# Optimization experiments

Measured on AMD Instinct MI355X. Metric: run time of the kernel, lower is better.

## Reference

```python
import jax, jax.numpy as jnp
import numpy as np

VOCAB, WORD_DIM, EMBED_SIZE, TENSOR_DIM, B = 100000, 300, 1024, 100, 16384

def leaky_relu(x):
    return jnp.where(x >= 0, x, 0.1 * x)

def setup_inputs() -> dict:
    key = jax.random.key(0)
    ks = jax.random.split(key, 12)
    H = EMBED_SIZE // 2
    def unif(k, shape, r):
        return jax.random.uniform(k, shape, jnp.float32, -r, r)
    def xavier_r(fan_in, fan_out):
        return float(np.sqrt(6.0) / np.sqrt(fan_in + fan_out))
    return {
        "x": jax.random.randint(ks[0], (B, 2), 0, VOCAB, dtype=jnp.int64) if jax.config.jax_enable_x64 else jax.random.randint(ks[0], (B, 2), 0, VOCAB, dtype=jnp.int32),
        "lengths": jnp.full((B,), 2, dtype=jnp.int32),
        "embed_W": unif(ks[1], (VOCAB, WORD_DIM), 0.1),
        "pd_W": unif(ks[2], (TENSOR_DIM, WORD_DIM), xavier_r(WORD_DIM, TENSOR_DIM)),
        "pd_b": jnp.zeros((TENSOR_DIM,), jnp.float32),
        "comp_T": jax.random.normal(ks[3], (TENSOR_DIM, 2 * TENSOR_DIM, 2 * TENSOR_DIM), jnp.float32),
        "cl_W": unif(ks[4], (TENSOR_DIM, 2 * TENSOR_DIM), xavier_r(2 * TENSOR_DIM, TENSOR_DIM)),
        "cl_b": jnp.zeros((TENSOR_DIM,), jnp.float32),
        "l1_W": unif(ks[5], (H, TENSOR_DIM), xavier_r(TENSOR_DIM, H)),
        "l1_b": jnp.zeros((H,), jnp.float32),
        "l2_W": unif(ks[6], (EMBED_SIZE, H), xavier_r(H, EMBED_SIZE)),
        "l2_b": jnp.zeros((EMBED_SIZE,), jnp.float32),
    }

def reference(x, lengths, embed_W, pd_W, pd_b, comp_T, cl_W, cl_b, l1_W, l1_b, l2_W, l2_b):
    # embedding lookup + projdown + leaky relu for att (x[:,0]) and obj (x[:,1])
    att = leaky_relu(embed_W[x[:, 0]] @ pd_W.T + pd_b)   # [B, T]
    obj = leaky_relu(embed_W[x[:, 1]] @ pd_W.T + pd_b)   # [B, T]
    cat = jnp.concatenate([att, obj], axis=1)            # [B, 2T]
    # fused trilinear form: cat^T . comp_T[k] . cat for all k at once
    term1 = jnp.einsum('bi,kij,bj->bk', cat, comp_T, cat)  # [B, T]
    term2 = cat @ cl_W.T + cl_b                            # [B, T]
    comp_vec = leaky_relu(term1 + term2)
    out = leaky_relu(comp_vec @ l1_W.T + l1_b) @ l2_W.T + l2_b  # [B, E]
    # l2norm over dim 1
    norm = jnp.sqrt(jnp.sum(out * out, axis=1, keepdims=True))
    return out / norm
```

## Files before the change

kernel.cpp:

```cpp
#include <hip/hip_runtime.h>
#include <hip/hip_bf16.h>

#define BATCH 16384
#define WDIM 300
#define TDIM 100
#define TD2 200
#define HDIM 512
#define ESIZE 1024

#define NIT 13
#define NJC 7
#define CSTR 232
#define CVSTR 136
#define HSTR 520

typedef unsigned short ush;
typedef float f32x2 __attribute__((ext_vector_type(2)));
typedef float f32x4 __attribute__((ext_vector_type(4)));
typedef _Float16 f16x8 __attribute__((ext_vector_type(8)));
typedef _Float16 f16x4 __attribute__((ext_vector_type(4)));

__device__ __forceinline__ float bf2f(ush u) {
    union { unsigned int i; float f; } v; v.i = ((unsigned int)u) << 16; return v.f;
}
__device__ __forceinline__ float2 bf2x2(unsigned int w) {
    union { unsigned int i; float f; } a, b;
    a.i = w << 16; b.i = w & 0xffff0000u;
    return make_float2(a.f, b.f);
}
__device__ __forceinline__ ush f2bf(float f) {
    union { float f; unsigned int i; } v; v.f = f;
    unsigned int x = v.i;
    return (ush)((x + 0x7fffu + ((x >> 16) & 1u)) >> 16);
}
__device__ __forceinline__ float leaky(float v) { return v >= 0.f ? v : 0.1f * v; }

__global__ __launch_bounds__(256) void kA3(const int* __restrict__ x,
                                           const float* __restrict__ eW,
                                           const float* __restrict__ pdW,
                                           const float* __restrict__ pdb,
                                           float* __restrict__ cat)
{
    __shared__ float eS[32][308];
    __shared__ float pS[20][308];
    __shared__ int idxS[32];
    const int tid = threadIdx.x;
    const int lane = tid & 63, wv = tid >> 6;
    const int b0 = blockIdx.x * 16;

    if (tid < 32) idxS[tid] = x[b0 * 2 + tid];
    __syncthreads();

    for (int r = wv; r < 32; r += 4) {
        const float4* src = (const float4*)(eW + (size_t)idxS[r] * WDIM);
        for (int d = lane; d < 75; d += 64) *(float4*)&eS[r][d * 4] = src[d];
    }

    const int r = tid >> 3, tl = tid & 7;
    const int t2ok = (tl + 16) < 20;
    const int b = b0 + (r >> 1), h = r & 1;

    for (int tc = 0; tc < 5; ++tc) {
        __syncthreads();
        for (int i = tid; i < 1500; i += 256) {
            int rr = i / 75, d = i - rr * 75;
            *(float4*)&pS[rr][d * 4] =
                *(const float4*)&pdW[(size_t)(tc * 20 + rr) * WDIM + d * 4];
        }
        __syncthreads();

        float a0 = 0.f, a1 = 0.f, a2 = 0.f;
        const int t2i = t2ok ? (tl + 16) : 0;
        for (int d = 0; d < 75; ++d) {
            float4 e4 = *(const float4*)&eS[r][d * 4];
            float4 p0 = *(const float4*)&pS[tl][d * 4];
            float4 p1 = *(const float4*)&pS[tl + 8][d * 4];
            float4 p2 = *(const float4*)&pS[t2i][d * 4];
            a0 += e4.x * p0.x + e4.y * p0.y + e4.z * p0.z + e4.w * p0.w;
            a1 += e4.x * p1.x + e4.y * p1.y + e4.z * p1.z + e4.w * p1.w;
            a2 += e4.x * p2.x + e4.y * p2.y + e4.z * p2.z + e4.w * p2.w;
        }
        {
            int t = tc * 20 + tl;
            cat[(size_t)b * TD2 + h * 100 + t] = leaky(a0 + pdb[t]);
            t += 8;
            cat[(size_t)b * TD2 + h * 100 + t] = leaky(a1 + pdb[t]);
            if (t2ok) {
                t += 8;
                cat[(size_t)b * TD2 + h * 100 + t] = leaky(a2 + pdb[t]);
            }
        }
    }
}

__global__ __launch_bounds__(448) void kT(const float* __restrict__ compT,
                                          const float* __restrict__ clW,
                                          ush* __restrict__ Tp)
{
    const int k = blockIdx.x, it = blockIdx.y;
    const int jc = threadIdx.x >> 6, lane = threadIdx.x & 63;
    const int i = it * 16 + (lane & 15);
    const int j0 = jc * 32 + (lane >> 4) * 8;
    ush vals[8];
    #pragma unroll
    for (int e = 0; e < 8; ++e) {
        int j = j0 + e;
        float v = 0.f;
        if (j < 200) {
            if (i < 200) v = compT[((size_t)k * 200 + i) * 200 + j];
            else if (i == 200) v = clW[(size_t)k * 200 + j];
        }
        union { _Float16 h; ush u; } cvt; cvt.h = (_Float16)v; vals[e] = cvt.u;
    }
    size_t o = (((size_t)k * NIT + it) * NJC + jc) * 64 + lane;
    ((uint4*)Tp)[o] = *(const uint4*)vals;
}

__global__ __launch_bounds__(256) void kW(const float* __restrict__ l1W,
                                          const float* __restrict__ l2W,
                                          ush* __restrict__ l1p,
                                          ush* __restrict__ l2p)
{
    const int idx = blockIdx.x * 256 + threadIdx.x;
    union { _Float16 h; ush u; } cvt;
    if (idx < HDIM * 128) {
        int r = idx >> 7, c = idx & 127;
        cvt.h = (_Float16)(c < TDIM ? l1W[r * TDIM + c] : 0.f);
        l1p[idx] = cvt.u;
    } else {
        int j = idx - HDIM * 128;
        cvt.h = (_Float16)l2W[j];
        l2p[j] = cvt.u;
    }
}

template<int NT>
__device__ __forceinline__ void kb7_work(const _Float16 (*__restrict__ cS)[CSTR],
                                         float (*__restrict__ pRed)[64],
                                         const ush* __restrict__ Tp,
                                         const float* __restrict__ clb,
                                         float* __restrict__ cv,
                                         int t0, int b0, int lane, int tid)
{
    const int cl = lane & 15, rg = lane >> 4;

    float cval[NT][4][4];
    #pragma unroll
    for (int it = 0; it < NT; ++it)
        #pragma unroll
        for (int bt = 0; bt < 4; ++bt)
            #pragma unroll
            for (int r = 0; r < 4; ++r)
                cval[it][bt][r] = (float)cS[bt * 16 + cl][(t0 + it) * 16 + rg * 4 + r];

    for (int k = 0; k < TDIM; ++k) {
        const int p = k & 1;
        f32x4 acc[NT][4];
        #pragma unroll
        for (int it = 0; it < NT; ++it)
            #pragma unroll
            for (int bt = 0; bt < 4; ++bt)
                acc[it][bt] = (f32x4){0.f, 0.f, 0.f, 0.f};

        #pragma unroll
        for (int jc = 0; jc < NJC; ++jc) {
            f16x8 ah[NT];
            #pragma unroll
            for (int it = 0; it < NT; ++it)
                ah[it] = *(const f16x8*)(Tp +
                    ((((size_t)k * NIT + (t0 + it)) * NJC + jc) * 64 + lane) * 8);
            f16x8 bh[4];
            #pragma unroll
            for (int bt = 0; bt < 4; ++bt)
                bh[bt] = *(const f16x8*)&cS[bt * 16 + cl][jc * 32 + rg * 8];
            #pragma unroll
            for (int it = 0; it < NT; ++it)
                #pragma unroll
                for (int bt = 0; bt < 4; ++bt)
                    acc[it][bt] = __builtin_amdgcn_mfma_f32_16x16x32_f16(
                        ah[it], bh[bt], acc[it][bt], 0, 0, 0);
        }
        #pragma unroll
        for (int bt = 0; bt < 4; ++bt) {
            float v = 0.f;
            #pragma unroll
            for (int it = 0; it < NT; ++it)
                #pragma unroll
                for (int r = 0; r < 4; ++r)
                    v += acc[it][bt][r] * cval[it][bt][r];
            v += __shfl_xor(v, 16);
            v += __shfl_xor(v, 32);
            if (lane < 16) atomicAdd(&pRed[p][bt * 16 + lane], v);
        }
        __syncthreads();
        if (tid < 64) {
            float s = pRed[p][tid];
            pRed[p][tid] = 0.f;
            cv[(size_t)k * BATCH + b0 + tid] = leaky(s + clb[k]);
        }
    }
}

__global__ __launch_bounds__(512, 2) void kB7(const float* __restrict__ cat,
                                              const ush* __restrict__ Tp,
                                              const float* __restrict__ clb,
                                              float* __restrict__ cv)
{
    __shared__ _Float16 cS[64][CSTR];
    __shared__ float pRed[2][64];
    const int tid = threadIdx.x;
    const int b0 = blockIdx.x * 64;
    const int lane = tid & 63, w = tid >> 6;

    for (int idx = tid; idx < 64 * CSTR; idx += 512) {
        int r = idx / CSTR, c = idx - r * CSTR;
        float v = 0.f;
        if (c < 200) v = cat[(size_t)(b0 + r) * TD2 + c];
        else if (c == 200) v = 1.f;
        cS[r][c] = (_Float16)v;
    }
    if (tid < 128) ((float*)pRed)[tid] = 0.f;
    __syncthreads();

    if (w < 5) kb7_work<2>(cS, pRed, Tp, clb, cv, 2 * w, b0, lane, tid);
    else       kb7_work<1>(cS, pRed, Tp, clb, cv, 10 + (w - 5), b0, lane, tid);
}

__global__ __launch_bounds__(512, 2) void kC1(const float* __restrict__ cv,
                                              const ush* __restrict__ l1p,
                                              const float* __restrict__ l1b,
                                              ush* __restrict__ h)
{
    __shared__ _Float16 cvS[64][CVSTR];
    const int tid = threadIdx.x;
    const int b0 = blockIdx.x * 64;
    const int lane = tid & 63, w = tid >> 6;
    const int cl = lane & 15, rg = lane >> 4;

    for (int k0 = 0; k0 < 128; k0 += 8) {
        int k = k0 + (w);
        int bl = lane;
        float v = (k < TDIM) ? cv[(size_t)k * BATCH + b0 + bl] : 0.f;
        cvS[bl][k] = (_Float16)v;
    }
    __syncthreads();

    for (int e8 = 0; e8 < 4; ++e8) {
        const int et = w * 4 + e8;
        f32x4 acc[4];
        #pragma unroll
        for (int bt = 0; bt < 4; ++bt) acc[bt] = (f32x4){0.f, 0.f, 0.f, 0.f};
        #pragma unroll
        for (int kc = 0; kc < 4; ++kc) {
            f16x8 a = *(const f16x8*)((const _Float16*)l1p +
                       (size_t)(et * 16 + cl) * 128 + kc * 32 + rg * 8);
            #pragma unroll
            for (int bt = 0; bt < 4; ++bt) {
                f16x8 b = *(const f16x8*)&cvS[bt * 16 + cl][kc * 32 + rg * 8];
                acc[bt] = __builtin_amdgcn_mfma_f32_16x16x32_f16(a, b, acc[bt], 0, 0, 0);
            }
        }
        float4 bias = *(const float4*)&l1b[et * 16 + rg * 4];
        #pragma unroll
        for (int bt = 0; bt < 4; ++bt) {
            f16x4 hv;
            hv[0] = (_Float16)leaky(acc[bt][0] + bias.x);
            hv[1] = (_Float16)leaky(acc[bt][1] + bias.y);
            hv[2] = (_Float16)leaky(acc[bt][2] + bias.z);
            hv[3] = (_Float16)leaky(acc[bt][3] + bias.w);
            *(f16x4*)((_Float16*)h + (size_t)(b0 + bt * 16 + cl) * HDIM
                      + et * 16 + rg * 4) = hv;
        }
    }
}

__global__ __launch_bounds__(512, 2) void kC2(const ush* __restrict__ h,
                                              const ush* __restrict__ l2p,
                                              const float* __restrict__ l2b,
                                              float* __restrict__ out,
                                              float* __restrict__ ssqg)
{
    __shared__ _Float16 hS[64][HSTR];
    __shared__ float ssqS[64];
    const int tid = threadIdx.x;
    const int b0 = blockIdx.x * 64;
    const int lane = tid & 63, w = tid >> 6;
    const int cl = lane & 15, rg = lane >> 4;

    for (int it = 0; it < 8; ++it) {
        int idx = it * 512 + tid;
        int row = idx >> 6, c8 = (idx & 63) * 8;
        *(uint4*)&hS[row][c8] = *(const uint4*)(h + (size_t)(b0 + row) * HDIM + c8);
    }
    if (tid < 64) ssqS[tid] = 0.f;
    __syncthreads();

    float ssqp[4] = {0.f, 0.f, 0.f, 0.f};
    for (int e8 = 0; e8 < 8; ++e8) {
        const int et = w * 8 + e8;
        f32x4 acc[4];
        #pragma unroll
        for (int bt = 0; bt < 4; ++bt) acc[bt] = (f32x4){0.f, 0.f, 0.f, 0.f};
        #pragma unroll
        for (int kc = 0; kc < 16; ++kc) {
            f16x8 a = *(const f16x8*)((const _Float16*)l2p +
                       (size_t)(et * 16 + cl) * HDIM + kc * 32 + rg * 8);
            #pragma unroll
            for (int bt = 0; bt < 4; ++bt) {
                f16x8 b = *(const f16x8*)&hS[bt * 16 + cl][kc * 32 + rg * 8];
                acc[bt] = __builtin_amdgcn_mfma_f32_16x16x32_f16(a, b, acc[bt], 0, 0, 0);
            }
        }
        float4 bias = *(const float4*)&l2b[et * 16 + rg * 4];
        #pragma unroll
        for (int bt = 0; bt < 4; ++bt) {
            float4 o;
            o.x = acc[bt][0] + bias.x;
            o.y = acc[bt][1] + bias.y;
            o.z = acc[bt][2] + bias.z;
            o.w = acc[bt][3] + bias.w;
            ssqp[bt] += o.x * o.x + o.y * o.y + o.z * o.z + o.w * o.w;
            *(float4*)&out[(size_t)(b0 + bt * 16 + cl) * ESIZE + et * 16 + rg * 4] = o;
        }
    }
    #pragma unroll
    for (int bt = 0; bt < 4; ++bt) {
        float s = ssqp[bt];
        s += __shfl_xor(s, 16);
        s += __shfl_xor(s, 32);
        if (lane < 16) atomicAdd(&ssqS[bt * 16 + lane], s);
    }
    __syncthreads();
    if (tid < 64) ssqg[b0 + tid] = ssqS[tid];
}

__global__ __launch_bounds__(512, 6) void kB4(const float* __restrict__ cat,
                                              const float* __restrict__ compT,
                                              const float* __restrict__ clW,
                                              const float* __restrict__ clb,
                                              float* __restrict__ cv)
{
    __shared__ float cS[64][201];
    const int tid = threadIdx.x;
    const int b0 = blockIdx.x * 64;
    const int lane = tid & 63;
    const int wid = tid >> 6;

    {
        int r = tid / TD2;
        int c = tid - r * TD2;
        for (int i = tid; i < 64 * TD2; i += 512) {
            cS[r][c] = cat[(size_t)(b0 + r) * TD2 + c];
            c += 112;
            if (c >= TD2) { c -= TD2; r += 3; } else { r += 2; }
        }
    }
    __syncthreads();

    int k = blockIdx.y * 8 + wid;
    if (k >= TDIM) return;
    k = __builtin_amdgcn_readfirstlane(k);

    const float* T = compT + (size_t)k * (TD2 * TD2);
    float s = 0.f;
    for (int ch = 0; ch < 4; ++ch) {
        const int c0 = ch * 50;
        f32x2 cj2[25];
        #pragma unroll
        for (int j = 0; j < 25; ++j) {
            f32x2 c2; c2.x = cS[lane][c0 + 2 * j]; c2.y = cS[lane][c0 + 2 * j + 1];
            cj2[j] = c2;
        }
        for (int i = 0; i < TD2; ++i) {
            const f32x2* T2 = (const f32x2*)(T + (size_t)i * TD2 + c0);
            f32x2 trow[25];
            #pragma unroll
            for (int j = 0; j < 25; ++j) trow[j] = T2[j];
            f32x2 u2; u2.x = 0.f; u2.y = 0.f;
            #pragma unroll
            for (int j = 0; j < 25; ++j) {
                asm("v_pk_fma_f32 %0, %1, %2, %0"
                    : "+v"(u2) : "s"(trow[j]), "v"(cj2[j]));
            }
            s += cS[lane][i] * (u2.x + u2.y);
        }
    }
    float t2 = 0.f;
    const float* W = clW + (size_t)k * TD2;
    for (int j = 0; j < TD2; ++j) t2 += W[j] * cS[lane][j];
    cv[(size_t)k * BATCH + b0 + lane] = leaky(s + t2 + clb[k]);
}

__global__ __launch_bounds__(256) void kCf(const float* __restrict__ cv,
                                           const float* __restrict__ l1W,
                                           const float* __restrict__ l1b,
                                           const float* __restrict__ l2W,
                                           const float* __restrict__ l2b,
                                           float* __restrict__ out,
                                           float* __restrict__ ssqg)
{
    __shared__ ush hS[32 * 528];
    __shared__ float w2F[8 * 516];
    const int tid = threadIdx.x;
    const int b0 = blockIdx.x * 32;

    float* cvS = w2F;
    for (int i = tid; i < 3200; i += 256) {
        int k = i >> 5, bl = i & 31;
        cvS[bl * TDIM + k] = cv[(size_t)k * BATCH + b0 + bl];
    }
    __syncthreads();
    for (int o = tid; o < 32 * HDIM; o += 256) {
        int bl = o & 31, e = o >> 5;
        const float* cr = &cvS[bl * TDIM];
        const float* wr = &l1W[e * TDIM];
        float s = 0.f;
        for (int t = 0; t < TDIM; t += 4) {
            float4 w4 = *(const float4*)&wr[t];
            float4 c4 = *(const float4*)&cr[t];
            s += w4.x * c4.x + w4.y * c4.y + w4.z * c4.z + w4.w * c4.w;
        }
        s = leaky(s + l1b[e]);
        hS[bl * 528 + e] = f2bf(s);
    }
    __syncthreads();

    const int b = tid >> 3, el = tid & 7;
    float ssq = 0.f;
    for (int ec = 0; ec < 128; ++ec) {
        {
            const float* src = l2W + (size_t)ec * 8 * HDIM;
            for (int i = tid; i < 1024; i += 256) {
                int r = i >> 7, c4 = (i & 127) * 4;
                *(float4*)&w2F[r * 516 + c4] = *(const float4*)&src[r * HDIM + c4];
            }
        }
        __syncthreads();
        {
            const ush* hr = &hS[b * 528];
            const float* wr2 = &w2F[el * 516];
            float s = 0.f;
            for (int j = 0; j < HDIM; j += 8) {
                uint4 hv = *(const uint4*)&hr[j];
                float4 w0 = *(const float4*)&wr2[j];
                float4 w1 = *(const float4*)&wr2[j + 4];
                float2 h0 = bf2x2(hv.x), h1 = bf2x2(hv.y), h2 = bf2x2(hv.z), h3 = bf2x2(hv.w);
                s += h0.x * w0.x + h0.y * w0.y + h1.x * w0.z + h1.y * w0.w
                   + h2.x * w1.x + h2.y * w1.y + h3.x * w1.z + h3.y * w1.w;
            }
            int eg = ec * 8 + el;
            float v = s + l2b[eg];
            out[(size_t)(b0 + b) * ESIZE + eg] = v;
            ssq += v * v;
        }
        __syncthreads();
    }
    ssq += __shfl_xor(ssq, 1);
    ssq += __shfl_xor(ssq, 2);
    ssq += __shfl_xor(ssq, 4);
    if (el == 0) ssqg[b0 + b] = ssq;
}

__global__ __launch_bounds__(256) void kD(float* __restrict__ out,
                                          const float* __restrict__ ssqg)
{
    const int tid = threadIdx.x;
    const int row = blockIdx.x * 2 + (tid >> 7);
    const int col = (tid & 127) * 8;
    const float r = rsqrtf(ssqg[row]);
    float* p = out + (size_t)row * ESIZE + col;
    float4 v0 = *(float4*)p;
    float4 v1 = *(float4*)(p + 4);
    v0.x *= r; v0.y *= r; v0.z *= r; v0.w *= r;
    v1.x *= r; v1.y *= r; v1.z *= r; v1.w *= r;
    *(float4*)p = v0;
    *(float4*)(p + 4) = v1;
}

extern "C" void kernel_launch(void* const* d_in, const int* in_sizes, int n_in,
                              void* d_out, int out_size, void* d_ws, size_t ws_size,
                              hipStream_t stream) {
    const int*   x    = (const int*)d_in[0];
    const float* eW   = (const float*)d_in[2];
    const float* pdW  = (const float*)d_in[3];
    const float* pdb  = (const float*)d_in[4];
    const float* cT   = (const float*)d_in[5];
    const float* clW  = (const float*)d_in[6];
    const float* clb  = (const float*)d_in[7];
    const float* l1W  = (const float*)d_in[8];
    const float* l1b  = (const float*)d_in[9];
    const float* l2W  = (const float*)d_in[10];
    const float* l2b  = (const float*)d_in[11];
    float* out = (float*)d_out;

    const size_t catN = (size_t)BATCH * TD2;
    const size_t cvN  = (size_t)BATCH * TDIM;
    const size_t ssqN = (size_t)BATCH;
    const size_t tpN  = (size_t)TDIM * NIT * NJC * 64 * 8;
    const size_t l1pN = (size_t)HDIM * 128;
    const size_t l2pN = (size_t)ESIZE * HDIM;
    const size_t hN   = (size_t)BATCH * HDIM;

    float* cat  = (float*)d_ws;
    float* cv   = cat + catN;
    float* ssqg = cv + cvN;
    ush*   Tp   = (ush*)(ssqg + ssqN);
    ush*   l1p  = Tp + tpN;
    ush*   l2p  = l1p + l1pN;
    ush*   hbuf = l2p + l2pN;

    const size_t need = (catN + cvN + ssqN) * 4 + (tpN + l1pN + l2pN + hN) * 2;

    kA3<<<dim3(BATCH / 16), dim3(256), 0, stream>>>(x, eW, pdW, pdb, cat);
    if (ws_size >= need) {
        kT <<<dim3(TDIM, NIT), dim3(448), 0, stream>>>(cT, clW, Tp);
        kW <<<dim3((HDIM * 128 + ESIZE * HDIM) / 256), dim3(256), 0, stream>>>(l1W, l2W, l1p, l2p);
        kB7<<<dim3(BATCH / 64), dim3(512), 0, stream>>>(cat, Tp, clb, cv);
        kC1<<<dim3(BATCH / 64), dim3(512), 0, stream>>>(cv, l1p, l1b, hbuf);
        kC2<<<dim3(BATCH / 64), dim3(512), 0, stream>>>(hbuf, l2p, l2b, out, ssqg);
    } else {
        kB4<<<dim3(BATCH / 64, 13), dim3(512), 0, stream>>>(cat, cT, clW, clb, cv);
        kCf<<<dim3(512), dim3(256), 0, stream>>>(cv, l1W, l1b, l2W, l2b, out, ssqg);
    }
    kD<<<dim3(8192), dim3(256), 0, stream>>>(out, ssqg);
}
```

Measured before the change: 846.2 us.

## Split trilinear kernel over k halves with partial-sum buffer and separate reduction

The bilinear kernel now splits the 100 output k-values between two blocks per batch tile. Within each block, warps are arranged as four i-tile groups times two k-lanes. Each warp writes its per-group partial sums to a global buffer, replacing the per-k shared-memory atomics and block-wide syncs. A new small kernel sums the four partials, adds the bias and applies leaky relu. Launch bounds rise to 4 blocks per SM for more occupancy, at the cost of a 26MB partial buffer round-trip, an extra launch, and cat values reread from LDS instead of held in registers.

```diff
diff --git a/kernel.cpp b/kernel.cpp
--- a/kernel.cpp
+++ b/kernel.cpp
@@ -135,26 +135,17 @@
 }
 
 template<int NT>
-__device__ __forceinline__ void kb7_work(const _Float16 (*__restrict__ cS)[CSTR],
-                                         float (*__restrict__ pRed)[64],
+__device__ __forceinline__ void kb8_work(const _Float16 (*__restrict__ cS)[CSTR],
                                          const ush* __restrict__ Tp,
-                                         const float* __restrict__ clb,
-                                         float* __restrict__ cv,
-                                         int t0, int b0, int lane, int tid)
+                                         float* __restrict__ part,
+                                         int t0, int q, int kq, int klane,
+                                         int b0, int lane)
 {
     const int cl = lane & 15, rg = lane >> 4;
-
-    float cval[NT][4][4];
-    #pragma unroll
-    for (int it = 0; it < NT; ++it)
-        #pragma unroll
-        for (int bt = 0; bt < 4; ++bt)
-            #pragma unroll
-            for (int r = 0; r < 4; ++r)
-                cval[it][bt][r] = (float)cS[bt * 16 + cl][(t0 + it) * 16 + rg * 4 + r];
-
-    for (int k = 0; k < TDIM; ++k) {
-        const int p = k & 1;
+    const int kbase = kq * 50;
+
+    for (int s = 0; s < 25; ++s) {
+        const int k = kbase + s * 2 + klane;
         f32x4 acc[NT][4];
         #pragma unroll
         for (int it = 0; it < NT; ++it)
@@ -184,32 +175,30 @@
         for (int bt = 0; bt < 4; ++bt) {
             float v = 0.f;
             #pragma unroll
-            for (int it = 0; it < NT; ++it)
-                #pragma unroll
-                for (int r = 0; r < 4; ++r)
-                    v += acc[it][bt][r] * cval[it][bt][r];
+            for (int it = 0; it < NT; ++it) {
+                f16x4 c4 = *(const f16x4*)&cS[bt * 16 + cl][(t0 + it) * 16 + rg * 4];
+                v += acc[it][bt][0] * (float)c4[0]
+                   + acc[it][bt][1] * (float)c4[1]
+                   + acc[it][bt][2] * (float)c4[2]
+                   + acc[it][bt][3] * (float)c4[3];
+            }
             v += __shfl_xor(v, 16);
             v += __shfl_xor(v, 32);
-            if (lane < 16) atomicAdd(&pRed[p][bt * 16 + lane], v);
-        }
-        __syncthreads();
-        if (tid < 64) {
-            float s = pRed[p][tid];
-            pRed[p][tid] = 0.f;
-            cv[(size_t)k * BATCH + b0 + tid] = leaky(s + clb[k]);
-        }
-    }
-}
-
-__global__ __launch_bounds__(512, 2) void kB7(const float* __restrict__ cat,
+            if (lane < 16)
+                part[((size_t)(q * TDIM + k) << 14) + b0 + bt * 16 + lane] = v;
+        }
+    }
+}
+
+__global__ __launch_bounds__(512, 4) void kB8(const float* __restrict__ cat,
                                               const ush* __restrict__ Tp,
-                                              const float* __restrict__ clb,
-                                              float* __restrict__ cv)
+                                              float* __restrict__ part)
 {
     __shared__ _Float16 cS[64][CSTR];
-    __shared__ float pRed[2][64];
-    const int tid = threadIdx.x;
-    const int b0 = blockIdx.x * 64;
+    const int tid = threadIdx.x;
+    const int bid = blockIdx.x;
+    const int kq = bid & 1;
+    const int b0 = (bid >> 1) * 64;
     const int lane = tid & 63, w = tid >> 6;
 
     for (int idx = tid; idx < 64 * CSTR; idx += 512) {
@@ -219,11 +208,27 @@
         else if (c == 200) v = 1.f;
         cS[r][c] = (_Float16)v;
     }
-    if (tid < 128) ((float*)pRed)[tid] = 0.f;
-    __syncthreads();
-
-    if (w < 5) kb7_work<2>(cS, pRed, Tp, clb, cv, 2 * w, b0, lane, tid);
-    else       kb7_work<1>(cS, pRed, Tp, clb, cv, 10 + (w - 5), b0, lane, tid);
+    __syncthreads();
+
+    const int q = w & 3, klane = w >> 2;
+    if (q == 0)      kb8_work<4>(cS, Tp, part, 0,  0, kq, klane, b0, lane);
+    else if (q == 1) kb8_work<3>(cS, Tp, part, 4,  1, kq, klane, b0, lane);
+    else if (q == 2) kb8_work<3>(cS, Tp, part, 7,  2, kq, klane, b0, lane);
+    else             kb8_work<3>(cS, Tp, part, 10, 3, kq, klane, b0, lane);
+}
+
+__global__ __launch_bounds__(256) void kB8b(const float* __restrict__ part,
+                                            const float* __restrict__ clb,
+                                            float* __restrict__ cv)
+{
+    const int idx = blockIdx.x * 256 + threadIdx.x;
+    const int b = idx & (BATCH - 1);
+    const int k = idx >> 14;
+    float s = part[((size_t)(0 * TDIM + k) << 14) + b]
+            + part[((size_t)(1 * TDIM + k) << 14) + b]
+            + part[((size_t)(2 * TDIM + k) << 14) + b]
+            + part[((size_t)(3 * TDIM + k) << 14) + b];
+    cv[(size_t)k * BATCH + b] = leaky(s + clb[k]);
 }
 
 __global__ __launch_bounds__(512, 2) void kC1(const float* __restrict__ cv,
@@ -496,6 +501,7 @@
     const size_t catN = (size_t)BATCH * TD2;
     const size_t cvN  = (size_t)BATCH * TDIM;
     const size_t ssqN = (size_t)BATCH;
+    const size_t partN = (size_t)4 * TDIM * BATCH;
     const size_t tpN  = (size_t)TDIM * NIT * NJC * 64 * 8;
     const size_t l1pN = (size_t)HDIM * 128;
     const size_t l2pN = (size_t)ESIZE * HDIM;
@@ -504,20 +510,22 @@
     float* cat  = (float*)d_ws;
     float* cv   = cat + catN;
     float* ssqg = cv + cvN;
-    ush*   Tp   = (ush*)(ssqg + ssqN);
+    float* part = ssqg + ssqN;
+    ush*   Tp   = (ush*)(part + partN);
     ush*   l1p  = Tp + tpN;
     ush*   l2p  = l1p + l1pN;
     ush*   hbuf = l2p + l2pN;
 
-    const size_t need = (catN + cvN + ssqN) * 4 + (tpN + l1pN + l2pN + hN) * 2;
+    const size_t need = (catN + cvN + ssqN + partN) * 4 + (tpN + l1pN + l2pN + hN) * 2;
 
     kA3<<<dim3(BATCH / 16), dim3(256), 0, stream>>>(x, eW, pdW, pdb, cat);
     if (ws_size >= need) {
-        kT <<<dim3(TDIM, NIT), dim3(448), 0, stream>>>(cT, clW, Tp);
-        kW <<<dim3((HDIM * 128 + ESIZE * HDIM) / 256), dim3(256), 0, stream>>>(l1W, l2W, l1p, l2p);
-        kB7<<<dim3(BATCH / 64), dim3(512), 0, stream>>>(cat, Tp, clb, cv);
-        kC1<<<dim3(BATCH / 64), dim3(512), 0, stream>>>(cv, l1p, l1b, hbuf);
-        kC2<<<dim3(BATCH / 64), dim3(512), 0, stream>>>(hbuf, l2p, l2b, out, ssqg);
+        kT  <<<dim3(TDIM, NIT), dim3(448), 0, stream>>>(cT, clW, Tp);
+        kW  <<<dim3((HDIM * 128 + ESIZE * HDIM) / 256), dim3(256), 0, stream>>>(l1W, l2W, l1p, l2p);
+        kB8 <<<dim3(BATCH / 64 * 2), dim3(512), 0, stream>>>(cat, Tp, part);
+        kB8b<<<dim3(BATCH * TDIM / 256), dim3(256), 0, stream>>>(part, clb, cv);
+        kC1 <<<dim3(BATCH / 64), dim3(512), 0, stream>>>(cv, l1p, l1b, hbuf);
+        kC2 <<<dim3(BATCH / 64), dim3(512), 0, stream>>>(hbuf, l2p, l2b, out, ssqg);
     } else {
         kB4<<<dim3(BATCH / 64, 13), dim3(512), 0, stream>>>(cat, cT, clW, clb, cv);
         kCf<<<dim3(512), dim3(256), 0, stream>>>(cv, l1W, l1b, l2W, l2b, out, ssqg);
```

Result: slower. 1.192 ms (+40.9%).
